# Performance work log

Hardware: AMD Instinct MI355X
Metric: run time of the kernel (lower is better)

The kernel has to match this reference:

```python
import jax, jax.numpy as jnp
import numpy as np

N = 50000
F_IN = 512
H1, C1 = 8, 16          # layer-1 heads / per-head channels
H2, C2 = 1, 40          # layer-2 heads / num_classes
NEG_SLOPE = 0.2


def setup_inputs() -> dict:
    key = jax.random.key(0)
    ks = jax.random.split(key, 10)
    E = 800000
    x = jax.random.normal(ks[0], (N, F_IN), dtype=jnp.float32)
    edge_index = jax.random.randint(ks[1], (2, E), 0, N, dtype=jnp.int64)
    s1 = 1.0 / np.sqrt(F_IN)
    s2 = 1.0 / np.sqrt(H1 * C1)
    return {
        "x": x,
        "edge_index": edge_index,
        "W1": jax.random.normal(ks[2], (F_IN, H1 * C1), dtype=jnp.float32) * s1,
        "att_src1": jax.random.normal(ks[3], (H1, C1), dtype=jnp.float32) * s2,
        "att_dst1": jax.random.normal(ks[4], (H1, C1), dtype=jnp.float32) * s2,
        "b1": jnp.zeros((H1 * C1,), dtype=jnp.float32),
        "W2": jax.random.normal(ks[5], (H1 * C1, H2 * C2), dtype=jnp.float32) * s2,
        "att_src2": jax.random.normal(ks[6], (H2, C2), dtype=jnp.float32) * (1.0 / np.sqrt(C2)),
        "att_dst2": jax.random.normal(ks[7], (H2, C2), dtype=jnp.float32) * (1.0 / np.sqrt(C2)),
        "b2": jnp.zeros((H2 * C2,), dtype=jnp.float32),
    }


def _gat_conv(x, W, att_src, att_dst, b, src, dst, H, C):
    # x: [N, Fin] -> h: [N, H, C]
    h = (x @ W).reshape(N, H, C)
    a_src = jnp.einsum("nhc,hc->nh", h, att_src)  # [N, H]
    a_dst = jnp.einsum("nhc,hc->nh", h, att_dst)
    e = a_src[src] + a_dst[dst]                    # [E, H]
    e = jax.nn.leaky_relu(e, NEG_SLOPE)
    # segment softmax over edges sharing the same target node (dst)
    m = jax.ops.segment_max(e, dst, num_segments=N)         # [N, H]
    ex = jnp.exp(e - m[dst])
    denom = jax.ops.segment_sum(ex, dst, num_segments=N)    # [N, H]
    alpha = ex / (denom[dst] + 1e-16)                        # [E, H]
    msg = h[src] * alpha[..., None]                          # [E, H, C]
    out = jax.ops.segment_sum(msg, dst, num_segments=N)     # [N, H, C]
    return out.reshape(N, H * C) + b


def reference(x, edge_index, W1, att_src1, att_dst1, b1, W2, att_src2, att_dst2, b2):
    # add self-loops (PyG GATConv default)
    loop = jnp.arange(N, dtype=edge_index.dtype)
    src = jnp.concatenate([edge_index[0], loop])
    dst = jnp.concatenate([edge_index[1], loop])
    h = _gat_conv(x, W1, att_src1, att_dst1, b1, src, dst, H1, C1)
    h = jax.nn.elu(h)
    h = _gat_conv(h, W2, att_src2, att_dst2, b2, src, dst, H2, C2)
    return jax.nn.log_softmax(h, axis=1)
```

## Files before the change

### kernel.cpp

```cpp
#include <hip/hip_runtime.h>
#include <math.h>

#define N_NODES 50000
#define FIN 512
#define NE 800000
#define ETOT 850000
#define F1 128
#define H1 8
#define F2 40
#define BCAP 64
#define NBIN 391
#define BINCAP 3072

typedef __attribute__((ext_vector_type(8))) short bf16x8;
typedef __attribute__((ext_vector_type(4))) float f32x4;

__device__ inline ushort f2bf(float f){
  union{float f; unsigned u;} v; v.f=f;
  return (ushort)((v.u + 0x8000u) >> 16);
}
__device__ inline float bflo(uint u){ union{uint a;float f;} v; v.a = u << 16;         return v.f; }
__device__ inline float bfhi(uint u){ union{uint a;float f;} v; v.a = u & 0xffff0000u; return v.f; }
__device__ inline float bf1(ushort u){ union{uint a;float f;} v; v.a = ((uint)u) << 16; return v.f; }

__device__ inline bf16x8 cvt8(float4 a, float4 b){
  union{ushort u[8]; bf16x8 v;} r;
  r.u[0]=f2bf(a.x); r.u[1]=f2bf(a.y); r.u[2]=f2bf(a.z); r.u[3]=f2bf(a.w);
  r.u[4]=f2bf(b.x); r.u[5]=f2bf(b.y); r.u[6]=f2bf(b.z); r.u[7]=f2bf(b.w);
  return r.v;
}


__global__ __launch_bounds__(1024) void k_pro(const int* __restrict__ src, const int* __restrict__ dst,
                                              int* __restrict__ binCursor, uint* __restrict__ binbuf,
                                              const float* __restrict__ W1, const float* __restrict__ W2,
                                              ushort* __restrict__ Wtb, ushort* __restrict__ Wt2){
  __shared__ int hist[512];
  __shared__ int base[512];
  int bx = blockIdx.x, t = threadIdx.x;

  if(bx < 104){
    if(t < 512) hist[t] = 0;
    __syncthreads();

    uint pk[8]; int bn[8];
    int i0 = bx*8192 + t;
    #pragma unroll
    for(int k=0;k<8;k++){
      int i = i0 + k*1024;
      int d = -1, s = 0;
      if(i < NE){ d = dst[i]; s = src[i]; }
      else if(i < ETOT){ d = i - NE; s = d; }
      if(d >= 0){
        bn[k] = d >> 7;
        pk[k] = ((uint)d << 16) | (uint)s;
        atomicAdd(&hist[bn[k]], 1);
      } else bn[k] = -1;
    }
    __syncthreads();
    if(t < 512){
      int h = hist[t];
      base[t] = (t < NBIN && h > 0) ? atomicAdd(&binCursor[t], h) : 0;
    }
    __syncthreads();
    if(t < 512) hist[t] = 0;
    __syncthreads();
    #pragma unroll
    for(int k=0;k<8;k++){
      if(bn[k] >= 0){
        int off = atomicAdd(&hist[bn[k]], 1);
        binbuf[(size_t)bn[k]*BINCAP + base[bn[k]] + off] = pk[k];
      }
    }
  } else {
    int id = (bx - 104)*1024 + t;
    if(id < 65536){
      int k = id >> 7, n = id & 127;
      Wtb[(size_t)(k>>3)*1024 + n*8 + (k&7)] = f2bf(W1[id]);
    } else {
      int id2 = id - 65536;
      if(id2 < 6144){
        int j = id2 & 7;
        int tt = id2 >> 3;
        int n = tt % 48;
        int t2 = tt / 48;
        int quad = t2 & 3, ks = t2 >> 2;
        int k = ks*32 + quad*8 + j;
        Wt2[id2] = (n < F2) ? f2bf(W2[k*F2 + n]) : (ushort)0;
      }
    }
  }
}


__global__ __launch_bounds__(256) void k_g1b(const int* __restrict__ binCursor, const uint* __restrict__ binbuf,
                                             int* __restrict__ cnt, ushort* __restrict__ bucket,
                                             const float* __restrict__ x, const ushort* __restrict__ Wtb,
                                             const float* __restrict__ as_w, const float* __restrict__ ad_w,
                                             ushort* __restrict__ h1b,
                                             float* __restrict__ a_src, float* __restrict__ a_dst){
  __shared__ __align__(16) char smem[17408];
  int bxg = blockIdx.x;

  if(bxg < NBIN){
    int* lcnt  = (int*)smem;
    ushort* lb = (ushort*)(smem + 512);
    int b = bxg, t = threadIdx.x;
    if(t < 128) lcnt[t] = 0;
    __syncthreads();
    int m = min(binCursor[b], BINCAP);
    const uint* p = binbuf + (size_t)b*BINCAP;
    for(int i=t; i<m; i+=256){
      uint pk = p[i];
      int dl = (pk >> 16) & 127;
      int pos = atomicAdd(&lcnt[dl], 1);
      if(pos < BCAP) lb[dl*66 + pos] = (ushort)(pk & 0xFFFF);
    }
    __syncthreads();
    int n0 = b << 7;
    int nrows = min(128, N_NODES - n0);
    if(t < nrows) cnt[n0 + t] = lcnt[t];
    const uint* s4 = (const uint*)(smem + 512);
    uint* d4 = (uint*)(bucket + ((size_t)n0 << 6));
    int total = nrows * 32;
    for(int i=t; i<total; i+=256){
      int r = i >> 5, c = i & 31;
      d4[i] = s4[r*33 + c];
    }
    return;
  }

  ushort* Asm = (ushort*)smem;
  int tid = threadIdx.x;
  int bx  = bxg - NBIN;
  int wave = tid >> 6, lane = tid & 63;
  int l15 = lane & 15, quad = lane >> 4;

  f32x4 acc[2][2];
  #pragma unroll
  for(int i=0;i<2;i++)
    #pragma unroll
    for(int j=0;j<2;j++) acc[i][j] = (f32x4){0.f,0.f,0.f,0.f};

  int am  = tid >> 3;
  int ak8 = (tid & 7) << 3;
  int agr = bx*32 + am;
  int agrc = min(agr, N_NODES-1);
  const float* xrow = x + (size_t)agrc*FIN + ak8;

  {
    float4 a0 = *(const float4*)xrow;
    float4 a1 = *(const float4*)(xrow + 4);
    *(bf16x8*)&Asm[am*72 + ak8] = cvt8(a0, a1);
  }

  const ushort* wpB = Wtb + (size_t)quad*1024 + (size_t)(wave*32 + l15)*8;

  bf16x8 bcur[2][2];
  #pragma unroll
  for(int ks=0;ks<2;ks++)
    #pragma unroll
    for(int tn=0;tn<2;tn++)
      bcur[ks][tn] = *(const bf16x8*)(wpB + ks*4096 + tn*128);
  __syncthreads();

  for(int kt=0; kt<FIN; kt+=64){
    int cur = (kt >> 6) & 1;
    bool hn = (kt + 64) < FIN;

    float4 a0, a1;
    if(hn){
      a0 = *(const float4*)(xrow + kt + 64);
      a1 = *(const float4*)(xrow + kt + 68);
    }
    bf16x8 bnext[2][2];
    if(hn){
      #pragma unroll
      for(int ks=0;ks<2;ks++)
        #pragma unroll
        for(int tn=0;tn<2;tn++)
          bnext[ks][tn] = *(const bf16x8*)(wpB + (size_t)(kt+64)*128 + ks*4096 + tn*128);
    }

    bf16x8 af[2][2];
    #pragma unroll
    for(int tm=0;tm<2;tm++)
      #pragma unroll
      for(int ks=0;ks<2;ks++)
        af[tm][ks] = *(bf16x8*)&Asm[cur*2304 + (tm*16 + l15)*72 + ks*32 + quad*8];

    #pragma unroll
    for(int ks=0;ks<2;ks++)
      #pragma unroll
      for(int tm=0;tm<2;tm++)
        #pragma unroll
        for(int tn=0;tn<2;tn++)
          acc[tm][tn] = __builtin_amdgcn_mfma_f32_16x16x32_bf16(af[tm][ks], bcur[ks][tn], acc[tm][tn], 0,0,0);

    if(hn)
      *(bf16x8*)&Asm[(cur^1)*2304 + am*72 + ak8] = cvt8(a0, a1);
    __syncthreads();
    #pragma unroll
    for(int ks=0;ks<2;ks++)
      #pragma unroll
      for(int tn=0;tn<2;tn++)
        bcur[ks][tn] = bnext[ks][tn];
  }

  float wsv[2], wdv[2];
  #pragma unroll
  for(int tn=0;tn<2;tn++){
    int h = wave*2 + tn;
    wsv[tn] = as_w[h*16 + l15];
    wdv[tn] = ad_w[h*16 + l15];
  }

  #pragma unroll
  for(int tm=0;tm<2;tm++){
    #pragma unroll
    for(int r=0;r<4;r++){
      int row = bx*32 + tm*16 + quad*4 + r;
      bool ok = row < N_NODES;
      #pragma unroll
      for(int tn=0;tn<2;tn++){
        float v = acc[tm][tn][r];
        if(ok){
          int col = wave*32 + tn*16 + l15;
          h1b[(size_t)row*F1 + col] = f2bf(v);
        }
        float ss = v * wsv[tn];
        float dd = v * wdv[tn];
        #pragma unroll
        for(int m=8;m;m>>=1){ ss += __shfl_xor(ss, m); dd += __shfl_xor(dd, m); }
        if(ok && l15 == 0){
          int h = wave*2 + tn;
          a_src[(size_t)row*H1 + h] = ss;
          a_dst[(size_t)row*H1 + h] = dd;
        }
      }
    }
  }
}


__global__ __launch_bounds__(256) void k_agg1(const ushort* __restrict__ h1b, const float* __restrict__ a_src,
                                              const float* __restrict__ a_dst,
                                              const int* __restrict__ cnt, const ushort* __restrict__ bucket,
                                              const float* __restrict__ b1, ushort* __restrict__ gb){
  int wave = threadIdx.x >> 6, lane = threadIdx.x & 63;
  int n = blockIdx.x*4 + wave;
  if(n >= N_NODES) return;
  int hl = lane >> 3;
  float adv = a_dst[n*H1 + hl];
  int deg = min(cnt[n], BCAP);
  int sv = (int)bucket[(n << 6) + lane];
  const uint* h1u = (const uint*)h1b;

  float ws0=0.f, ax0=0.f, ay0=0.f;
  float ws1=0.f, ax1=0.f, ay1=0.f;
  float ws2=0.f, ax2=0.f, ay2=0.f;
  float ws3=0.f, ax3=0.f, ay3=0.f;
  int j = 0;
  for(; j+3<deg; j+=4){
    int s0 = __shfl(sv, j),   s1 = __shfl(sv, j+1);
    int s2 = __shfl(sv, j+2), s3 = __shfl(sv, j+3);
    float e0 = a_src[s0*H1 + hl] + adv;
    float e1 = a_src[s1*H1 + hl] + adv;
    float e2 = a_src[s2*H1 + hl] + adv;
    float e3 = a_src[s3*H1 + hl] + adv;
    e0 = e0 > 0.f ? e0 : 0.2f*e0;  e1 = e1 > 0.f ? e1 : 0.2f*e1;
    e2 = e2 > 0.f ? e2 : 0.2f*e2;  e3 = e3 > 0.f ? e3 : 0.2f*e3;
    float w0=__expf(e0), w1=__expf(e1), w2=__expf(e2), w3=__expf(e3);
    uint u0 = h1u[(size_t)s0*64 + lane];
    uint u1 = h1u[(size_t)s1*64 + lane];
    uint u2 = h1u[(size_t)s2*64 + lane];
    uint u3 = h1u[(size_t)s3*64 + lane];
    ax0 += w0*bflo(u0); ay0 += w0*bfhi(u0); ws0 += w0;
    ax1 += w1*bflo(u1); ay1 += w1*bfhi(u1); ws1 += w1;
    ax2 += w2*bflo(u2); ay2 += w2*bfhi(u2); ws2 += w2;
    ax3 += w3*bflo(u3); ay3 += w3*bfhi(u3); ws3 += w3;
  }
  for(; j<deg; j++){
    int s0 = __shfl(sv, j);
    float e0 = a_src[s0*H1 + hl] + adv;
    e0 = e0 > 0.f ? e0 : 0.2f*e0;
    float w0 = __expf(e0);
    uint u0 = h1u[(size_t)s0*64 + lane];
    ax0 += w0*bflo(u0); ay0 += w0*bfhi(u0); ws0 += w0;
  }
  float wsum = (ws0+ws1)+(ws2+ws3);
  float inv = 1.f/(wsum + 1e-16f);
  int c0 = lane*2;
  float o0 = ((ax0+ax1)+(ax2+ax3))*inv + b1[c0];
  float o1 = ((ay0+ay1)+(ay2+ay3))*inv + b1[c0+1];
  o0 = o0 > 0.f ? o0 : expm1f(o0);
  o1 = o1 > 0.f ? o1 : expm1f(o1);
  uint up = (uint)f2bf(o0) | ((uint)f2bf(o1) << 16);
  ((uint*)gb)[(size_t)n*64 + lane] = up;
}


__global__ __launch_bounds__(256) void k_gemm2(const ushort* __restrict__ gb, const ushort* __restrict__ Wt2,
                                               const float* __restrict__ as_w, const float* __restrict__ ad_w,
                                               ushort* __restrict__ h2b,
                                               float* __restrict__ a_src, float* __restrict__ a_dst){
  int tid = threadIdx.x;
  int wave = tid >> 6, lane = tid & 63;
  int l15 = lane & 15, quad = lane >> 4;
  int row0 = blockIdx.x*64 + wave*16;
  int arow = min(row0 + l15, N_NODES-1);
  const ushort* ap = gb + (size_t)arow*F1 + quad*8;

  f32x4 acc[3];
  #pragma unroll
  for(int tn=0;tn<3;tn++) acc[tn] = (f32x4){0.f,0.f,0.f,0.f};

  #pragma unroll
  for(int ks=0;ks<4;ks++){
    bf16x8 af = *(const bf16x8*)(ap + ks*32);
    #pragma unroll
    for(int tn=0;tn<3;tn++){
      bf16x8 bf = *(const bf16x8*)(Wt2 + ((size_t)(ks*4+quad)*48 + tn*16 + l15)*8);
      acc[tn] = __builtin_amdgcn_mfma_f32_16x16x32_bf16(af, bf, acc[tn], 0,0,0);
    }
  }

  float ws2v[3], wd2v[3];
  #pragma unroll
  for(int tn=0;tn<3;tn++){
    int col = tn*16 + l15;
    ws2v[tn] = (col < F2) ? as_w[col] : 0.f;
    wd2v[tn] = (col < F2) ? ad_w[col] : 0.f;
  }

  #pragma unroll
  for(int r=0;r<4;r++){
    int row = row0 + quad*4 + r;
    bool ok = row < N_NODES;
    float ss = 0.f, dd = 0.f;
    #pragma unroll
    for(int tn=0;tn<3;tn++){
      float v = acc[tn][r];
      int col = tn*16 + l15;
      if(ok && col < F2) h2b[(size_t)row*F2 + col] = f2bf(v);
      ss += v * ws2v[tn];
      dd += v * wd2v[tn];
    }
    #pragma unroll
    for(int m=8;m;m>>=1){ ss += __shfl_xor(ss, m); dd += __shfl_xor(dd, m); }
    if(ok && l15 == 0){
      a_src[row] = ss;
      a_dst[row] = dd;
    }
  }
}


__global__ __launch_bounds__(256) void k_agg2(const ushort* __restrict__ h2b, const float* __restrict__ a_src,
                                              const float* __restrict__ a_dst,
                                              const int* __restrict__ cnt, const ushort* __restrict__ bucket,
                                              const float* __restrict__ b2, float* __restrict__ out){
  int wave = threadIdx.x >> 6, lane = threadIdx.x & 63;
  int n = blockIdx.x*4 + wave;
  if(n >= N_NODES) return;
  float adv = a_dst[n];
  int deg = min(cnt[n], BCAP);
  int sv = (int)bucket[(n << 6) + lane];
  int c = (lane < F2) ? lane : (F2-1);

  float ws0=0.f, ac0=0.f, ws1=0.f, ac1=0.f, ws2=0.f, ac2=0.f, ws3=0.f, ac3=0.f;
  int j = 0;
  for(; j+3<deg; j+=4){
    int s0 = __shfl(sv, j),   s1 = __shfl(sv, j+1);
    int s2 = __shfl(sv, j+2), s3 = __shfl(sv, j+3);
    float e0 = a_src[s0] + adv, e1 = a_src[s1] + adv;
    float e2 = a_src[s2] + adv, e3 = a_src[s3] + adv;
    e0 = e0 > 0.f ? e0 : 0.2f*e0;  e1 = e1 > 0.f ? e1 : 0.2f*e1;
    e2 = e2 > 0.f ? e2 : 0.2f*e2;  e3 = e3 > 0.f ? e3 : 0.2f*e3;
    float w0=__expf(e0), w1=__expf(e1), w2=__expf(e2), w3=__expf(e3);
    ac0 += w0*bf1(h2b[(size_t)s0*F2 + c]); ws0 += w0;
    ac1 += w1*bf1(h2b[(size_t)s1*F2 + c]); ws1 += w1;
    ac2 += w2*bf1(h2b[(size_t)s2*F2 + c]); ws2 += w2;
    ac3 += w3*bf1(h2b[(size_t)s3*F2 + c]); ws3 += w3;
  }
  for(; j<deg; j++){
    int s0 = __shfl(sv, j);
    float e0 = a_src[s0] + adv;
    e0 = e0 > 0.f ? e0 : 0.2f*e0;
    float w0 = __expf(e0);
    ac0 += w0*bf1(h2b[(size_t)s0*F2 + c]); ws0 += w0;
  }
  float v = ((ac0+ac1)+(ac2+ac3))/(((ws0+ws1)+(ws2+ws3)) + 1e-16f) + b2[c];
  float mv = (lane < F2) ? v : -INFINITY;
  #pragma unroll
  for(int off=32; off; off>>=1) mv = fmaxf(mv, __shfl_xor(mv, off));
  float ex = (lane < F2) ? __expf(v - mv) : 0.f;
  #pragma unroll
  for(int off=32; off; off>>=1) ex += __shfl_xor(ex, off);
  if(lane < F2) out[(size_t)n*F2 + lane] = v - mv - logf(ex);
}


extern "C" void kernel_launch(void* const* d_in, const int* in_sizes, int n_in,
                              void* d_out, int out_size, void* d_ws, size_t ws_size,
                              hipStream_t stream) {
  const float* x        = (const float*)d_in[0];
  const int*   eidx     = (const int*)d_in[1];
  const float* W1       = (const float*)d_in[2];
  const float* att_src1 = (const float*)d_in[3];
  const float* att_dst1 = (const float*)d_in[4];
  const float* b1       = (const float*)d_in[5];
  const float* W2       = (const float*)d_in[6];
  const float* att_src2 = (const float*)d_in[7];
  const float* att_dst2 = (const float*)d_in[8];
  const float* b2       = (const float*)d_in[9];
  float* out = (float*)d_out;

  const int* src = eidx;
  const int* dst = eidx + NE;

  ushort* h1b  = (ushort*)d_ws;
  ushort* h2b  = h1b + 6400000;
  ushort* gb   = h2b + 2000000;
  ushort* Wtb  = gb + 6400000;
  ushort* bucket = Wtb + 65536;
  float* a_src1 = (float*)(bucket + 3200000);
  float* a_dst1 = a_src1 + 400000;
  float* a_src2 = a_dst1 + 400000;
  float* a_dst2 = a_src2 + 50000;
  int* cnt      = (int*)(a_dst2 + 50000);
  int* binCursor= cnt + 50002;
  uint* binbuf  = (uint*)(binCursor + 512);
  ushort* Wt2   = (ushort*)(binbuf + (size_t)NBIN*BINCAP);

  hipMemsetAsync(binCursor, 0, 512*sizeof(int), stream);

  k_pro<<<174, 1024, 0, stream>>>(src, dst, binCursor, binbuf, W1, W2, Wtb, Wt2);

  k_g1b<<<NBIN + 1563, 256, 0, stream>>>(binCursor, binbuf, cnt, bucket,
                                         x, Wtb, att_src1, att_dst1, h1b, a_src1, a_dst1);

  k_agg1<<<(N_NODES+3)/4, 256, 0, stream>>>(h1b, a_src1, a_dst1, cnt, bucket, b1, gb);

  k_gemm2<<<(N_NODES+63)/64, 256, 0, stream>>>(gb, Wt2, att_src2, att_dst2, h2b, a_src2, a_dst2);
  k_agg2 <<<(N_NODES+3)/4, 256, 0, stream>>>(h2b, a_src2, a_dst2, cnt, bucket, b2, out);
}
```

Measured before the change: 281.7 us.

## Load GEMM A fragments directly from global memory, dropping LDS staging

The layer-1 projection GEMM no longer stages x tiles through double-buffered shared memory with per-iteration barriers. Each wave instead loads its own MFMA A fragments straight from global memory and converts them to bf16 in registers, and the explicit register prefetch of B fragments is removed. This eliminates LDS writes and reads and the __syncthreads per k-step. In exchange, each of the 4 waves redundantly reads the same x rows from global/L2, and the software pipelining that overlapped loads with MFMAs is gone.

```diff
diff --git a/kernel.cpp b/kernel.cpp
--- a/kernel.cpp
+++ b/kernel.cpp
@@ -130,7 +130,6 @@
     return;
   }
 
-  ushort* Asm = (ushort*)smem;
   int tid = threadIdx.x;
   int bx  = bxg - NBIN;
   int wave = tid >> 6, lane = tid & 63;
@@ -142,52 +141,35 @@
     #pragma unroll
     for(int j=0;j<2;j++) acc[i][j] = (f32x4){0.f,0.f,0.f,0.f};
 
-  int am  = tid >> 3;
-  int ak8 = (tid & 7) << 3;
-  int agr = bx*32 + am;
-  int agrc = min(agr, N_NODES-1);
-  const float* xrow = x + (size_t)agrc*FIN + ak8;
-
-  {
-    float4 a0 = *(const float4*)xrow;
-    float4 a1 = *(const float4*)(xrow + 4);
-    *(bf16x8*)&Asm[am*72 + ak8] = cvt8(a0, a1);
-  }
+  int r0 = min(bx*32 + l15,      N_NODES-1);
+  int r1 = min(bx*32 + 16 + l15, N_NODES-1);
+  const float* xr0 = x + (size_t)r0*FIN + quad*8;
+  const float* xr1 = x + (size_t)r1*FIN + quad*8;
 
   const ushort* wpB = Wtb + (size_t)quad*1024 + (size_t)(wave*32 + l15)*8;
 
-  bf16x8 bcur[2][2];
-  #pragma unroll
-  for(int ks=0;ks<2;ks++)
-    #pragma unroll
-    for(int tn=0;tn<2;tn++)
-      bcur[ks][tn] = *(const bf16x8*)(wpB + ks*4096 + tn*128);
-  __syncthreads();
-
   for(int kt=0; kt<FIN; kt+=64){
-    int cur = (kt >> 6) & 1;
-    bool hn = (kt + 64) < FIN;
-
-    float4 a0, a1;
-    if(hn){
-      a0 = *(const float4*)(xrow + kt + 64);
-      a1 = *(const float4*)(xrow + kt + 68);
-    }
-    bf16x8 bnext[2][2];
-    if(hn){
+    float4 a000 = *(const float4*)(xr0 + kt);
+    float4 a001 = *(const float4*)(xr0 + kt + 4);
+    float4 a010 = *(const float4*)(xr0 + kt + 32);
+    float4 a011 = *(const float4*)(xr0 + kt + 36);
+    float4 a100 = *(const float4*)(xr1 + kt);
+    float4 a101 = *(const float4*)(xr1 + kt + 4);
+    float4 a110 = *(const float4*)(xr1 + kt + 32);
+    float4 a111 = *(const float4*)(xr1 + kt + 36);
+
+    bf16x8 bfr[2][2];
+    #pragma unroll
+    for(int ks=0;ks<2;ks++)
       #pragma unroll
-      for(int ks=0;ks<2;ks++)
-        #pragma unroll
-        for(int tn=0;tn<2;tn++)
-          bnext[ks][tn] = *(const bf16x8*)(wpB + (size_t)(kt+64)*128 + ks*4096 + tn*128);
-    }
+      for(int tn=0;tn<2;tn++)
+        bfr[ks][tn] = *(const bf16x8*)(wpB + (size_t)kt*128 + ks*4096 + tn*128);
 
     bf16x8 af[2][2];
-    #pragma unroll
-    for(int tm=0;tm<2;tm++)
-      #pragma unroll
-      for(int ks=0;ks<2;ks++)
-        af[tm][ks] = *(bf16x8*)&Asm[cur*2304 + (tm*16 + l15)*72 + ks*32 + quad*8];
+    af[0][0] = cvt8(a000, a001);
+    af[0][1] = cvt8(a010, a011);
+    af[1][0] = cvt8(a100, a101);
+    af[1][1] = cvt8(a110, a111);
 
     #pragma unroll
     for(int ks=0;ks<2;ks++)
@@ -195,16 +177,7 @@
       for(int tm=0;tm<2;tm++)
         #pragma unroll
         for(int tn=0;tn<2;tn++)
-          acc[tm][tn] = __builtin_amdgcn_mfma_f32_16x16x32_bf16(af[tm][ks], bcur[ks][tn], acc[tm][tn], 0,0,0);
-
-    if(hn)
-      *(bf16x8*)&Asm[(cur^1)*2304 + am*72 + ak8] = cvt8(a0, a1);
-    __syncthreads();
-    #pragma unroll
-    for(int ks=0;ks<2;ks++)
-      #pragma unroll
-      for(int tn=0;tn<2;tn++)
-        bcur[ks][tn] = bnext[ks][tn];
+          acc[tm][tn] = __builtin_amdgcn_mfma_f32_16x16x32_bf16(af[tm][ks], bfr[ks][tn], acc[tm][tn], 0,0,0);
   }
 
   float wsv[2], wdv[2];
```

Result: slower. 308.7 us (+9.6%).
